# Kernel tuning notes

Measured on AMD Instinct MI355X. Metric: run time of the kernel, lower is better.

The kernel has to match this reference:

```python
import jax, jax.numpy as jnp
import numpy as np

NUM_CLASSES = 100
EPS = 1e-07


def setup_inputs() -> dict:
    key = jax.random.key(0)
    k1, k2 = jax.random.split(key)
    N = 1_000_000
    logits = jax.random.normal(k1, (N, NUM_CLASSES), dtype=jnp.float32)
    labels = jax.random.randint(k2, (N,), 0, NUM_CLASSES, dtype=jnp.int32)
    return {"logits": logits, "labels": labels}


def reference(logits, labels):
    # pred: [N] argmax class per sample
    pred = jnp.argmax(logits, axis=1)
    C = NUM_CLASSES
    zeros = jnp.zeros((C,), dtype=jnp.float32)
    # single-pass confusion-matrix marginals (replaces per-class python loop)
    pred_count = zeros.at[pred].add(1.0)          # tp_c + fp_c
    true_count = zeros.at[labels].add(1.0)        # tp_c + fn_c
    correct = (pred == labels).astype(jnp.float32)
    tp = zeros.at[labels].add(correct)            # tp_c
    fp = pred_count - tp
    fn = true_count - tp
    precision = tp / (tp + fp + EPS)
    recall = tp / (tp + fn + EPS)
    # beta = 1 -> (1 + 1) * p * r / (1 * p + r + eps)
    f1 = 2.0 * precision * recall / (precision + recall + EPS)
    return jnp.mean(f1)
```

## Files before the change

kernel.cpp:

```cpp
#include <hip/hip_runtime.h>

#define NCLS 100
#define EPS 1e-7f
#define ROWS_PER_BLOCK 512
#define N_ITER (ROWS_PER_BLOCK / 64)

__global__ void zero_counts_kernel(unsigned int* __restrict__ counts) {
    int i = threadIdx.x;
    if (i < 3 * NCLS) counts[i] = 0u;
}

__device__ __forceinline__ void load7(const float4* __restrict__ f4,
                                      int r, int q, int rowEnd,
                                      float4 v[7], int* lab,
                                      const int* __restrict__ labels) {
    if (r < rowEnd) {
        const size_t A = ((size_t)r * 25) & ~(size_t)3;
        #pragma unroll
        for (int k = 0; k < 7; ++k) v[k] = f4[A + 4 * k + q];
        if (q == 0) *lab = labels[r];
    }
}

__device__ __forceinline__ void process7(const float4 v[7], int r, int q,
                                         int rowEnd, int lab,
                                         unsigned int* s_pred,
                                         unsigned int* s_true,
                                         unsigned int* s_tp) {
    float best = -INFINITY;
    int bidx = 0;
    if (r < rowEnd) {
        const int r3 = r & 3;
        const int off = (q - r3) << 2;
        #pragma unroll
        for (int k = 0; k < 7; ++k) {
            const int cb = 16 * k + off;
            float4 w = v[k];
            if ((unsigned)(cb + 0) < (unsigned)NCLS && w.x > best) { best = w.x; bidx = cb;     }
            if ((unsigned)(cb + 1) < (unsigned)NCLS && w.y > best) { best = w.y; bidx = cb + 1; }
            if ((unsigned)(cb + 2) < (unsigned)NCLS && w.z > best) { best = w.z; bidx = cb + 2; }
            if ((unsigned)(cb + 3) < (unsigned)NCLS && w.w > best) { best = w.w; bidx = cb + 3; }
        }
    }
    #pragma unroll
    for (int m = 1; m <= 2; m <<= 1) {
        float ob = __shfl_xor(best, m, 64);
        int   oi = __shfl_xor(bidx, m, 64);
        if (ob > best || (ob == best && oi < bidx)) { best = ob; bidx = oi; }
    }
    if (q == 0 && r < rowEnd) {
        atomicAdd(&s_pred[bidx], 1u);
        atomicAdd(&s_true[lab], 1u);
        if (bidx == lab) atomicAdd(&s_tp[lab], 1u);
    }
}

__global__ __launch_bounds__(256) void hist_kernel(
        const float* __restrict__ logits,
        const int* __restrict__ labels,
        unsigned int* __restrict__ counts,
        int N) {
    __shared__ unsigned int s_pred[NCLS];
    __shared__ unsigned int s_true[NCLS];
    __shared__ unsigned int s_tp[NCLS];
    for (int i = threadIdx.x; i < NCLS; i += blockDim.x) {
        s_pred[i] = 0u; s_true[i] = 0u; s_tp[i] = 0u;
    }
    __syncthreads();

    const int lane = threadIdx.x & 63;
    const int wv   = threadIdx.x >> 6;
    const int q    = lane & 3;
    const int g    = lane >> 2;

    const int blockStart = blockIdx.x * ROWS_PER_BLOCK;
    const int rowEnd     = min(blockStart + ROWS_PER_BLOCK, N);

    const float4* f4 = (const float4*)logits;

    int row = blockStart + wv * 16 + g;

    float4 va[7], vb[7];
    int la = 0, lb = 0;

    load7(f4, row, q, rowEnd, va, &la, labels);

    #pragma unroll 1
    for (int i = 0; i < N_ITER; i += 2) {
        const int r1 = row + 64;
        load7(f4, r1, q, rowEnd, vb, &lb, labels);
        process7(va, row, q, rowEnd, la, s_pred, s_true, s_tp);

        const int r2 = r1 + 64;
        if (i + 2 < N_ITER) {
            load7(f4, r2, q, rowEnd, va, &la, labels);
        }
        process7(vb, r1, q, rowEnd, lb, s_pred, s_true, s_tp);

        row = r2;
    }

    __syncthreads();
    for (int i = threadIdx.x; i < NCLS; i += blockDim.x) {
        unsigned int v;
        if ((v = s_pred[i]) != 0u) atomicAdd(&counts[i], v);
        if ((v = s_true[i]) != 0u) atomicAdd(&counts[NCLS + i], v);
        if ((v = s_tp[i])   != 0u) atomicAdd(&counts[2 * NCLS + i], v);
    }
}

__global__ void finalize_kernel(const unsigned int* __restrict__ counts,
                                float* __restrict__ out) {
    __shared__ float s_f1[NCLS];
    int c = threadIdx.x;
    if (c < NCLS) {
        float tp    = (float)counts[2 * NCLS + c];
        float predc = (float)counts[c];
        float truec = (float)counts[NCLS + c];
        float fp = predc - tp;
        float fn = truec - tp;
        float precision = tp / (tp + fp + EPS);
        float recall    = tp / (tp + fn + EPS);
        float f1 = 2.0f * precision * recall / (precision + recall + EPS);
        s_f1[c] = f1;
    }
    __syncthreads();
    if (c == 0) {
        float sum = 0.0f;
        for (int i = 0; i < NCLS; ++i) sum += s_f1[i];
        out[0] = sum / (float)NCLS;
    }
}

extern "C" void kernel_launch(void* const* d_in, const int* in_sizes, int n_in,
                              void* d_out, int out_size, void* d_ws, size_t ws_size,
                              hipStream_t stream) {
    const float* logits = (const float*)d_in[0];
    const int*   labels = (const int*)d_in[1];
    float* out = (float*)d_out;
    unsigned int* counts = (unsigned int*)d_ws;

    const int N = in_sizes[1];

    zero_counts_kernel<<<1, 320, 0, stream>>>(counts);

    const int block = 256;
    const int grid  = (N + ROWS_PER_BLOCK - 1) / ROWS_PER_BLOCK;
    hist_kernel<<<grid, block, 0, stream>>>(logits, labels, counts, N);

    finalize_kernel<<<1, 128, 0, stream>>>(counts, out);
}
```

Before: 528.1 us.

## Load each 16-row window contiguously and reduce argmax via shared 64-bit atomicMax

New measurement: 562.7 us. 6.6% more time.

```diff
diff --git a/kernel.cpp b/kernel.cpp
--- a/kernel.cpp
+++ b/kernel.cpp
@@ -10,48 +10,61 @@
     if (i < 3 * NCLS) counts[i] = 0u;
 }
 
-__device__ __forceinline__ void load7(const float4* __restrict__ f4,
-                                      int r, int q, int rowEnd,
-                                      float4 v[7], int* lab,
-                                      const int* __restrict__ labels) {
-    if (r < rowEnd) {
-        const size_t A = ((size_t)r * 25) & ~(size_t)3;
-        #pragma unroll
-        for (int k = 0; k < 7; ++k) v[k] = f4[A + 4 * k + q];
-        if (q == 0) *lab = labels[r];
+__device__ __forceinline__ void loadwin(const float4* __restrict__ f4,
+                                        const int* __restrict__ labels,
+                                        int rowBase, int rowEnd, int lane,
+                                        float4 v[7], int* lab) {
+    const int rows = rowEnd - rowBase;
+    if (rows <= 0) return;
+    const int maxj = (rows >= 16) ? 400 : rows * 25;
+    const size_t base = (size_t)rowBase * 25;
+    #pragma unroll
+    for (int k = 0; k < 7; ++k) {
+        const int j = 64 * k + lane;
+        if (j < maxj) v[k] = f4[base + j];
     }
+    if (lane < 16 && lane < rows) *lab = labels[rowBase + lane];
 }
 
-__device__ __forceinline__ void process7(const float4 v[7], int r, int q,
-                                         int rowEnd, int lab,
-                                         unsigned int* s_pred,
-                                         unsigned int* s_true,
-                                         unsigned int* s_tp) {
-    float best = -INFINITY;
-    int bidx = 0;
-    if (r < rowEnd) {
-        const int r3 = r & 3;
-        const int off = (q - r3) << 2;
-        #pragma unroll
-        for (int k = 0; k < 7; ++k) {
-            const int cb = 16 * k + off;
-            float4 w = v[k];
-            if ((unsigned)(cb + 0) < (unsigned)NCLS && w.x > best) { best = w.x; bidx = cb;     }
-            if ((unsigned)(cb + 1) < (unsigned)NCLS && w.y > best) { best = w.y; bidx = cb + 1; }
-            if ((unsigned)(cb + 2) < (unsigned)NCLS && w.z > best) { best = w.z; bidx = cb + 2; }
-            if ((unsigned)(cb + 3) < (unsigned)NCLS && w.w > best) { best = w.w; bidx = cb + 3; }
+__device__ __forceinline__ void procwin(const float4 v[7],
+                                        int rowBase, int rowEnd,
+                                        int lane, int lab,
+                                        unsigned long long* __restrict__ s_win,
+                                        unsigned int* __restrict__ s_pred,
+                                        unsigned int* __restrict__ s_true,
+                                        unsigned int* __restrict__ s_tp) {
+    const int rows = rowEnd - rowBase;
+    if (rows <= 0) return;
+    const int maxj = (rows >= 16) ? 400 : rows * 25;
+
+    if (lane < 16) s_win[lane] = 0ull;
+
+    #pragma unroll
+    for (int k = 0; k < 7; ++k) {
+        const int j = 64 * k + lane;
+        if (j < maxj) {
+            const int rl = j / 25;
+            const int fq = j - rl * 25;
+            const int cb = fq << 2;
+            const float4 w = v[k];
+            float bv = w.x; int bc = cb;
+            if (w.y > bv) { bv = w.y; bc = cb + 1; }
+            if (w.z > bv) { bv = w.z; bc = cb + 2; }
+            if (w.w > bv) { bv = w.w; bc = cb + 3; }
+            unsigned ku = __float_as_uint(bv);
+            ku = (ku & 0x80000000u) ? ~ku : (ku | 0x80000000u);
+            const unsigned long long pk =
+                ((unsigned long long)ku << 32) | (unsigned)(127 - bc);
+            atomicMax(&s_win[rl], pk);
         }
     }
-    #pragma unroll
-    for (int m = 1; m <= 2; m <<= 1) {
-        float ob = __shfl_xor(best, m, 64);
-        int   oi = __shfl_xor(bidx, m, 64);
-        if (ob > best || (ob == best && oi < bidx)) { best = ob; bidx = oi; }
-    }
-    if (q == 0 && r < rowEnd) {
-        atomicAdd(&s_pred[bidx], 1u);
+
+    if (lane < 16 && lane < rows) {
+        const unsigned long long pk = s_win[lane];
+        const int col = 127 - (int)(pk & 0xFFull);
+        atomicAdd(&s_pred[col], 1u);
         atomicAdd(&s_true[lab], 1u);
-        if (bidx == lab) atomicAdd(&s_tp[lab], 1u);
+        if (col == lab) atomicAdd(&s_tp[lab], 1u);
     }
 }
 
@@ -63,6 +76,7 @@
     __shared__ unsigned int s_pred[NCLS];
     __shared__ unsigned int s_true[NCLS];
     __shared__ unsigned int s_tp[NCLS];
+    __shared__ unsigned long long s_win[4][16];
     for (int i = threadIdx.x; i < NCLS; i += blockDim.x) {
         s_pred[i] = 0u; s_true[i] = 0u; s_tp[i] = 0u;
     }
@@ -70,34 +84,32 @@
 
     const int lane = threadIdx.x & 63;
     const int wv   = threadIdx.x >> 6;
-    const int q    = lane & 3;
-    const int g    = lane >> 2;
 
     const int blockStart = blockIdx.x * ROWS_PER_BLOCK;
     const int rowEnd     = min(blockStart + ROWS_PER_BLOCK, N);
 
     const float4* f4 = (const float4*)logits;
 
-    int row = blockStart + wv * 16 + g;
+    int rowBase = blockStart + wv * 16;
 
     float4 va[7], vb[7];
     int la = 0, lb = 0;
 
-    load7(f4, row, q, rowEnd, va, &la, labels);
+    loadwin(f4, labels, rowBase, rowEnd, lane, va, &la);
 
     #pragma unroll 1
     for (int i = 0; i < N_ITER; i += 2) {
-        const int r1 = row + 64;
-        load7(f4, r1, q, rowEnd, vb, &lb, labels);
-        process7(va, row, q, rowEnd, la, s_pred, s_true, s_tp);
+        const int r1 = rowBase + 64;
+        loadwin(f4, labels, r1, rowEnd, lane, vb, &lb);
+        procwin(va, rowBase, rowEnd, lane, la, s_win[wv], s_pred, s_true, s_tp);
 
         const int r2 = r1 + 64;
         if (i + 2 < N_ITER) {
-            load7(f4, r2, q, rowEnd, va, &la, labels);
+            loadwin(f4, labels, r2, rowEnd, lane, va, &la);
         }
-        process7(vb, r1, q, rowEnd, lb, s_pred, s_true, s_tp);
+        procwin(vb, r1, rowEnd, lane, lb, s_win[wv], s_pred, s_true, s_tp);
 
-        row = r2;
+        rowBase = r2;
     }
 
     __syncthreads();
```
